# Optimization experiments

Hardware: AMD Instinct MI355X
Metric: run time of the kernel (lower is better)

The kernel has to match this reference:

```python
import jax, jax.numpy as jnp
import numpy as np

N = 100000   # num_embeddings
D = 128      # embedding_dims
E = 128      # edge_output_size
S = 2048     # number of streaming interactions
W_DECAY = 1.0  # Decayer w, decay_method='exp': f(dt) = exp(-w*dt)


def setup_inputs() -> dict:
    key = jax.random.key(0)
    ks = jax.random.split(key, 20)
    def nrm(k, shape, s):
        return jax.random.normal(k, shape, jnp.float32) * s
    sD = 1.0 / np.sqrt(D)
    sE = 1.0 / np.sqrt(E)
    return {
        'heads': jax.random.randint(ks[0], (S,), 0, N, dtype=jnp.int32),
        'tails': jax.random.randint(ks[1], (S,), 0, N, dtype=jnp.int32),
        'times': jnp.sort(jax.random.uniform(ks[2], (S,), jnp.float32) * 100.0),
        # node state tables (nn.Embedding weights in the original)
        'node_rep': nrm(ks[3], (N, D), 0.1),
        'cell_head': nrm(ks[4], (N, D), 0.1),
        'hidden_head': nrm(ks[5], (N, D), 0.1),
        'cell_tail': nrm(ks[6], (N, D), 0.1),
        'hidden_tail': nrm(ks[7], (N, D), 0.1),
        # Edge_updater_nn head / tail: act(rep_h @ W1 + rep_t @ W2 + b)
        'Weh1': nrm(ks[8], (D, E), sD), 'Weh2': nrm(ks[9], (D, E), sD), 'beh': jnp.zeros((E,), jnp.float32),
        'Wet1': nrm(ks[10], (D, E), sD), 'Wet2': nrm(ks[11], (D, E), sD), 'bet': jnp.zeros((E,), jnp.float32),
        # TLSTM head (time-decayed LSTM cell)
        'Wxh': nrm(ks[12], (E, 4 * D), sE), 'Whh': nrm(ks[13], (D, 4 * D), sD), 'bh': jnp.zeros((4 * D,), jnp.float32),
        'Wdh': nrm(ks[14], (D, D), sD), 'bdh': jnp.zeros((D,), jnp.float32),
        # TLSTM tail
        'Wxt': nrm(ks[15], (E, 4 * D), sE), 'Wht': nrm(ks[16], (D, 4 * D), sD), 'bt': jnp.zeros((4 * D,), jnp.float32),
        'Wdt': nrm(ks[17], (D, D), sD), 'bdt': jnp.zeros((D,), jnp.float32),
        # Combiner: tanh(h_head @ Wc1 + h_tail @ Wc2)
        'Wc1': nrm(ks[18], (D, D), sD), 'Wc2': nrm(ks[19], (D, D), sD),
    }


def _tlstm(x, c, h, decay, Wx, Wh, b, Wd, bd):
    # Time-aware LSTM: decompose short-term memory, decay it by elapsed time, recombine.
    cs = jnp.tanh(c @ Wd + bd)      # short-term memory component
    c_adj = c - cs + cs * decay      # adjusted previous cell
    z = x @ Wx + h @ Wh + b          # [4D] gate pre-activations
    i, f, o, g = jnp.split(z, 4)
    i = jax.nn.sigmoid(i); f = jax.nn.sigmoid(f); o = jax.nn.sigmoid(o)
    g = jnp.tanh(g)
    c_new = f * c_adj + i * g
    h_new = o * jnp.tanh(c_new)
    return c_new, h_new


def reference(heads, tails, times, node_rep, cell_head, hidden_head, cell_tail, hidden_tail,
              Weh1, Weh2, beh, Wet1, Wet2, bet,
              Wxh, Whh, bh, Wdh, bdh, Wxt, Wht, bt, Wdt, bdt, Wc1, Wc2):
    recent = jnp.zeros((node_rep.shape[0],), jnp.float32)  # recent_timestamp, init 0

    def step(state, ev):
        rep, ch, hh, ct, ht, rt = state
        h_i, t_i, tm = ev
        rep_h = rep[h_i]                    # gather current reps
        rep_t = rep[t_i]
        dec_h = jnp.exp(-W_DECAY * (tm - rt[h_i]))   # decayer(delta_t)
        dec_t = jnp.exp(-W_DECAY * (tm - rt[t_i]))
        edge_h = jnp.tanh(rep_h @ Weh1 + rep_t @ Weh2 + beh)  # edge_updater_head
        edge_t = jnp.tanh(rep_h @ Wet1 + rep_t @ Wet2 + bet)  # edge_updater_tail
        c_h, h_h = _tlstm(edge_h, ch[h_i], hh[h_i], dec_h, Wxh, Whh, bh, Wdh, bdh)
        c_t, h_t = _tlstm(edge_t, ct[t_i], ht[t_i], dec_t, Wxt, Wht, bt, Wdt, bdt)
        new_rep_h = jnp.tanh(h_h @ Wc1 + ht[h_i] @ Wc2)  # combiner(head hidden, tail hidden)
        new_rep_t = jnp.tanh(hh[t_i] @ Wc1 + h_t @ Wc2)
        # scatter updated state (head written before tail, matching original ordering)
        rep = rep.at[h_i].set(new_rep_h).at[t_i].set(new_rep_t)
        ch = ch.at[h_i].set(c_h); hh = hh.at[h_i].set(h_h)
        ct = ct.at[t_i].set(c_t); ht = ht.at[t_i].set(h_t)
        rt = rt.at[h_i].set(tm).at[t_i].set(tm)
        # if_updated=0: emit pre-update representations for this interaction
        return (rep, ch, hh, ct, ht, rt), (rep_h, rep_t)

    state0 = (node_rep, cell_head, hidden_head, cell_tail, hidden_tail, recent)
    _, (out_h, out_t) = jax.lax.scan(step, state0, (heads, tails, times))
    return jnp.stack([out_h, out_t])  # [2, S, D]
```

## Files before the change

### kernel.cpp

```cpp
#include <hip/hip_runtime.h>
#include <hip/hip_cooperative_groups.h>
#include <math.h>

namespace cg = cooperative_groups;

#define NBLK 256
#define DD 128
#define SMAX 2048

__device__ __forceinline__ float sigmoidf(float x) { return 1.0f / (1.0f + expf(-x)); }

__global__ __launch_bounds__(1024) void schedule_kernel(
    const int* __restrict__ heads, const int* __restrict__ tails, int S,
    int* __restrict__ order, int* __restrict__ level_off, int* __restrict__ n_levels) {
  __shared__ int sh[SMAX], st[SMAX], lvl[SMAX], ph[SMAX], pt[SMAX], cnt[SMAX];
  __shared__ int changed, maxl;
  const int tid = threadIdx.x;

  for (int j = tid; j < S; j += 1024) { sh[j] = heads[j]; st[j] = tails[j]; }
  __syncthreads();

  for (int r = 0; r < 2; ++r) {
    int j = (r == 0) ? tid : (2047 - tid);
    if (j < S && (r == 0 ? (tid < 1024) : (2047 - tid >= 1024))) {
      int myh = sh[j], myt = st[j];
      int mph = -1, mpt = -1;
      for (int i = 0; i < j; ++i) {
        int a = sh[i], b = st[i];
        if (a == myh || b == myh) mph = i;
        if (a == myt || b == myt) mpt = i;
      }
      ph[j] = mph; pt[j] = mpt; lvl[j] = 1;
    }
  }
  __syncthreads();

  for (int it = 0; it < S + 2; ++it) {
    __syncthreads();
    if (tid == 0) changed = 0;
    __syncthreads();
    for (int j = tid; j < S; j += 1024) {
      int l = 1;
      int a = ph[j]; if (a >= 0) l = lvl[a] + 1;
      int b = pt[j]; if (b >= 0) { int lb = lvl[b] + 1; if (lb > l) l = lb; }
      if (l != lvl[j]) { lvl[j] = l; changed = 1; }
    }
    __syncthreads();
    if (!changed) break;
  }

  if (tid == 0) maxl = 0;
  __syncthreads();
  for (int j = tid; j < S; j += 1024) atomicMax(&maxl, lvl[j]);
  __syncthreads();
  const int M = maxl;

  for (int l = tid; l < M; l += 1024) cnt[l] = 0;
  __syncthreads();
  for (int j = tid; j < S; j += 1024) atomicAdd(&cnt[lvl[j] - 1], 1);
  __syncthreads();
  if (tid == 0) {
    int run = 0;
    level_off[0] = 0;
    for (int l = 0; l < M; ++l) { run += cnt[l]; level_off[l + 1] = run; }
    n_levels[0] = M;
  }
  __syncthreads();

  for (int l = tid; l < M; l += 1024) cnt[l] = 0;
  __syncthreads();
  for (int j = tid; j < S; j += 1024) {
    int lv = lvl[j] - 1;
    int pos = level_off[lv] + atomicAdd(&cnt[lv], 1);
    order[pos] = j;
  }
}

struct PParams {
  const int* heads; const int* tails; const float* times;
  float* node_rep; float* cell_head; float* hidden_head; float* cell_tail; float* hidden_tail;
  const float* Weh1; const float* Weh2; const float* beh;
  const float* Wet1; const float* Wet2; const float* bet;
  const float* Wxh; const float* Whh; const float* bh; const float* Wdh; const float* bdh;
  const float* Wxt; const float* Wht; const float* bt; const float* Wdt; const float* bdt;
  const float* Wc1; const float* Wc2;
  float* out; float* rt;
  const int* order; const int* level_off; const int* n_levels;
  int S;
};

__global__ __launch_bounds__(256) void process_kernel(PParams p) {
  cg::grid_group grid = cg::this_grid();
  const int tid = threadIdx.x;

  __shared__ float repH[DD], repT[DD], cHs[DD], hHs[DD], cTs[DD], hTs[DD];
  __shared__ float htH[DD], hhT[DD];
  __shared__ float edgeH[DD], edgeT[DD], cadjH[DD], cadjT[DD];
  __shared__ float zH[512], zT[512];
  __shared__ float nhH[DD], nhT[DD];
  __shared__ float dec2[2], tmS;
  __shared__ int idx2[2];

  const int nlv = p.n_levels[0];
  for (int lv = 0; lv < nlv; ++lv) {
    const int beg = p.level_off[lv], end = p.level_off[lv + 1];
    for (int k = beg + blockIdx.x; k < end; k += gridDim.x) {
      __syncthreads();
      const int s = p.order[k];
      if (tid == 0) { idx2[0] = p.heads[s]; idx2[1] = p.tails[s]; tmS = p.times[s]; }
      __syncthreads();
      const int hI = idx2[0], tI = idx2[1];
      const float tm = tmS;
      if (tid < 2) dec2[tid] = expf(-(tm - p.rt[idx2[tid]]));

      if (tid < DD) {
        const int d = tid;
        const size_t o = (size_t)hI * DD + d;
        float r = p.node_rep[o];
        repH[d] = r; cHs[d] = p.cell_head[o]; hHs[d] = p.hidden_head[o];
        htH[d] = p.hidden_tail[o];
        p.out[(size_t)s * DD + d] = r;
      } else {
        const int d = tid - DD;
        const size_t o = (size_t)tI * DD + d;
        float r = p.node_rep[o];
        repT[d] = r; cTs[d] = p.cell_tail[o]; hTs[d] = p.hidden_tail[o];
        hhT[d] = p.hidden_head[o];
        p.out[(size_t)(p.S + s) * DD + d] = r;
      }
      __syncthreads();

      if (tid < DD) {
        const int e = tid;
        float ae = p.beh[e], ac = p.bdh[e];
#pragma unroll 4
        for (int d = 0; d < DD; ++d) {
          ae += repH[d] * p.Weh1[d * DD + e] + repT[d] * p.Weh2[d * DD + e];
          ac += cHs[d] * p.Wdh[d * DD + e];
        }
        edgeH[e] = tanhf(ae);
        float cs = tanhf(ac);
        cadjH[e] = cHs[e] - cs + cs * dec2[0];
      } else {
        const int e = tid - DD;
        float ae = p.bet[e], ac = p.bdt[e];
#pragma unroll 4
        for (int d = 0; d < DD; ++d) {
          ae += repH[d] * p.Wet1[d * DD + e] + repT[d] * p.Wet2[d * DD + e];
          ac += cTs[d] * p.Wdt[d * DD + e];
        }
        edgeT[e] = tanhf(ae);
        float cs = tanhf(ac);
        cadjT[e] = cTs[e] - cs + cs * dec2[1];
      }
      __syncthreads();

      {
        float a0 = p.bh[tid], a1 = p.bh[tid + 256];
        float b0 = p.bt[tid], b1 = p.bt[tid + 256];
#pragma unroll 2
        for (int d = 0; d < DD; ++d) {
          const float eh = edgeH[d], hh = hHs[d], et = edgeT[d], ht = hTs[d];
          a0 += eh * p.Wxh[d * 512 + tid]       + hh * p.Whh[d * 512 + tid];
          a1 += eh * p.Wxh[d * 512 + tid + 256] + hh * p.Whh[d * 512 + tid + 256];
          b0 += et * p.Wxt[d * 512 + tid]       + ht * p.Wht[d * 512 + tid];
          b1 += et * p.Wxt[d * 512 + tid + 256] + ht * p.Wht[d * 512 + tid + 256];
        }
        zH[tid] = a0; zH[tid + 256] = a1;
        zT[tid] = b0; zT[tid + 256] = b1;
      }
      __syncthreads();

      if (tid < DD) {
        const int e = tid;
        float ig = sigmoidf(zH[e]), fg = sigmoidf(zH[DD + e]);
        float og = sigmoidf(zH[256 + e]), gg = tanhf(zH[384 + e]);
        float c = fg * cadjH[e] + ig * gg;
        float h = og * tanhf(c);
        nhH[e] = h;
        p.cell_head[(size_t)hI * DD + e] = c;
        p.hidden_head[(size_t)hI * DD + e] = h;
      } else {
        const int e = tid - DD;
        float ig = sigmoidf(zT[e]), fg = sigmoidf(zT[DD + e]);
        float og = sigmoidf(zT[256 + e]), gg = tanhf(zT[384 + e]);
        float c = fg * cadjT[e] + ig * gg;
        float h = og * tanhf(c);
        nhT[e] = h;
        p.cell_tail[(size_t)tI * DD + e] = c;
        p.hidden_tail[(size_t)tI * DD + e] = h;
      }
      if (tid == 0) p.rt[hI] = tm;
      if (tid == 1) p.rt[tI] = tm;
      __syncthreads();

      if (tid < DD) {
        const int e = tid;
        float a = 0.f;
#pragma unroll 4
        for (int d = 0; d < DD; ++d)
          a += nhH[d] * p.Wc1[d * DD + e] + htH[d] * p.Wc2[d * DD + e];
        if (hI != tI) p.node_rep[(size_t)hI * DD + e] = tanhf(a);
      } else {
        const int e = tid - DD;
        float a = 0.f;
#pragma unroll 4
        for (int d = 0; d < DD; ++d)
          a += hhT[d] * p.Wc1[d * DD + e] + nhT[d] * p.Wc2[d * DD + e];
        p.node_rep[(size_t)tI * DD + e] = tanhf(a);
      }
    }
    __threadfence();
    grid.sync();
  }
}

extern "C" void kernel_launch(void* const* d_in, const int* in_sizes, int n_in,
                              void* d_out, int out_size, void* d_ws, size_t ws_size,
                              hipStream_t stream) {
  const int* heads = (const int*)d_in[0];
  const int* tails = (const int*)d_in[1];
  const float* times = (const float*)d_in[2];
  float* node_rep    = (float*)d_in[3];
  float* cell_head   = (float*)d_in[4];
  float* hidden_head = (float*)d_in[5];
  float* cell_tail   = (float*)d_in[6];
  float* hidden_tail = (float*)d_in[7];
  const float* Weh1 = (const float*)d_in[8];
  const float* Weh2 = (const float*)d_in[9];
  const float* beh  = (const float*)d_in[10];
  const float* Wet1 = (const float*)d_in[11];
  const float* Wet2 = (const float*)d_in[12];
  const float* bet  = (const float*)d_in[13];
  const float* Wxh  = (const float*)d_in[14];
  const float* Whh  = (const float*)d_in[15];
  const float* bh   = (const float*)d_in[16];
  const float* Wdh  = (const float*)d_in[17];
  const float* bdh  = (const float*)d_in[18];
  const float* Wxt  = (const float*)d_in[19];
  const float* Wht  = (const float*)d_in[20];
  const float* bt   = (const float*)d_in[21];
  const float* Wdt  = (const float*)d_in[22];
  const float* bdt  = (const float*)d_in[23];
  const float* Wc1  = (const float*)d_in[24];
  const float* Wc2  = (const float*)d_in[25];

  const int S = in_sizes[0];
  const int N = in_sizes[3] / DD;

  char* ws = (char*)d_ws;
  float* rt = (float*)ws;
  size_t rtBytes = (((size_t)N * 4) + 511) & ~(size_t)511;
  int* order     = (int*)(ws + rtBytes);
  int* level_off = order + SMAX;
  int* n_levels  = level_off + SMAX + 1;

  hipMemsetAsync(rt, 0, (size_t)N * 4, stream);
  schedule_kernel<<<1, 1024, 0, stream>>>(heads, tails, S, order, level_off, n_levels);

  PParams p;
  p.heads = heads; p.tails = tails; p.times = times;
  p.node_rep = node_rep; p.cell_head = cell_head; p.hidden_head = hidden_head;
  p.cell_tail = cell_tail; p.hidden_tail = hidden_tail;
  p.Weh1 = Weh1; p.Weh2 = Weh2; p.beh = beh;
  p.Wet1 = Wet1; p.Wet2 = Wet2; p.bet = bet;
  p.Wxh = Wxh; p.Whh = Whh; p.bh = bh; p.Wdh = Wdh; p.bdh = bdh;
  p.Wxt = Wxt; p.Wht = Wht; p.bt = bt; p.Wdt = Wdt; p.bdt = bdt;
  p.Wc1 = Wc1; p.Wc2 = Wc2;
  p.out = (float*)d_out; p.rt = rt;
  p.order = order; p.level_off = level_off; p.n_levels = n_levels;
  p.S = S;

  void* args[] = { (void*)&p };
  hipLaunchCooperativeKernel((const void*)process_kernel, dim3(NBLK), dim3(256),
                             args, 0, stream);
}
```

Before: 808.2 us.

## Parallelize predecessor search across blocks and size cooperative grid by occupancy

The O(S^2) predecessor search used to run inside a single 1024-thread block. It now runs in its own kernel with one 64-lane wavefront per interaction and a shuffle max-reduction. Level propagation moves into a separate finalize kernel that reads the predecessors from workspace. The cooperative process kernel's grid is now sized from CU count and occupancy, up to 1024 blocks, with fallbacks, so more interactions per level can run concurrently. This adds an extra kernel launch and host occupancy queries on every call.

```diff
diff --git a/kernel.cpp b/kernel.cpp
--- a/kernel.cpp
+++ b/kernel.cpp
@@ -4,39 +4,44 @@
 
 namespace cg = cooperative_groups;
 
-#define NBLK 256
+#define NBLK_MAX 1024
 #define DD 128
 #define SMAX 2048
 
 __device__ __forceinline__ float sigmoidf(float x) { return 1.0f / (1.0f + expf(-x)); }
 
-__global__ __launch_bounds__(1024) void schedule_kernel(
+__global__ __launch_bounds__(64) void pred_kernel(
     const int* __restrict__ heads, const int* __restrict__ tails, int S,
+    int* __restrict__ ph, int* __restrict__ pt) {
+  const int j = blockIdx.x;
+  if (j >= S) return;
+  const int myh = heads[j], myt = tails[j];
+  const int lane = threadIdx.x;
+  int mph = -1, mpt = -1;
+  for (int i = lane; i < j; i += 64) {
+    int a = heads[i], b = tails[i];
+    if (a == myh || b == myh) mph = i;
+    if (a == myt || b == myt) mpt = i;
+  }
+#pragma unroll
+  for (int off = 32; off > 0; off >>= 1) {
+    mph = max(mph, __shfl_down(mph, off));
+    mpt = max(mpt, __shfl_down(mpt, off));
+  }
+  if (lane == 0) { ph[j] = mph; pt[j] = mpt; }
+}
+
+__global__ __launch_bounds__(1024) void finalize_kernel(
+    int S, const int* __restrict__ phg, const int* __restrict__ ptg,
     int* __restrict__ order, int* __restrict__ level_off, int* __restrict__ n_levels) {
-  __shared__ int sh[SMAX], st[SMAX], lvl[SMAX], ph[SMAX], pt[SMAX], cnt[SMAX];
+  __shared__ int lvl[SMAX], ph[SMAX], pt[SMAX], cnt[SMAX];
   __shared__ int changed, maxl;
   const int tid = threadIdx.x;
 
-  for (int j = tid; j < S; j += 1024) { sh[j] = heads[j]; st[j] = tails[j]; }
-  __syncthreads();
-
-  for (int r = 0; r < 2; ++r) {
-    int j = (r == 0) ? tid : (2047 - tid);
-    if (j < S && (r == 0 ? (tid < 1024) : (2047 - tid >= 1024))) {
-      int myh = sh[j], myt = st[j];
-      int mph = -1, mpt = -1;
-      for (int i = 0; i < j; ++i) {
-        int a = sh[i], b = st[i];
-        if (a == myh || b == myh) mph = i;
-        if (a == myt || b == myt) mpt = i;
-      }
-      ph[j] = mph; pt[j] = mpt; lvl[j] = 1;
-    }
-  }
+  for (int j = tid; j < S; j += 1024) { ph[j] = phg[j]; pt[j] = ptg[j]; lvl[j] = 1; }
   __syncthreads();
 
   for (int it = 0; it < S + 2; ++it) {
-    __syncthreads();
     if (tid == 0) changed = 0;
     __syncthreads();
     for (int j = tid; j < S; j += 1024) {
@@ -47,6 +52,7 @@
     }
     __syncthreads();
     if (!changed) break;
+    __syncthreads();
   }
 
   if (tid == 0) maxl = 0;
@@ -101,7 +107,9 @@
   __shared__ float dec2[2], tmS;
   __shared__ int idx2[2];
 
-  const int nlv = p.n_levels[0];
+  int nlv = p.n_levels[0];
+  if (nlv < 0) nlv = 0;
+  if (nlv > SMAX) nlv = SMAX;
   for (int lv = 0; lv < nlv; ++lv) {
     const int beg = p.level_off[lv], end = p.level_off[lv + 1];
     for (int k = beg + blockIdx.x; k < end; k += gridDim.x) {
@@ -254,9 +262,12 @@
   int* order     = (int*)(ws + rtBytes);
   int* level_off = order + SMAX;
   int* n_levels  = level_off + SMAX + 1;
+  int* ph        = n_levels + 64;
+  int* pt        = ph + SMAX;
 
   hipMemsetAsync(rt, 0, (size_t)N * 4, stream);
-  schedule_kernel<<<1, 1024, 0, stream>>>(heads, tails, S, order, level_off, n_levels);
+  pred_kernel<<<S, 64, 0, stream>>>(heads, tails, S, ph, pt);
+  finalize_kernel<<<1, 1024, 0, stream>>>(S, ph, pt, order, level_off, n_levels);
 
   PParams p;
   p.heads = heads; p.tails = tails; p.times = times;
@@ -272,6 +283,24 @@
   p.S = S;
 
   void* args[] = { (void*)&p };
-  hipLaunchCooperativeKernel((const void*)process_kernel, dim3(NBLK), dim3(256),
-                             args, 0, stream);
+
+  int dev = 0; hipGetDevice(&dev);
+  int nCU = 0;
+  hipDeviceGetAttribute(&nCU, hipDeviceAttributeMultiprocessorCount, dev);
+  if (nCU <= 0) nCU = 256;
+  int maxBlkPerCU = 0;
+  hipOccupancyMaxActiveBlocksPerMultiprocessor(&maxBlkPerCU, process_kernel, 256, 0);
+  if (maxBlkPerCU < 1) maxBlkPerCU = 1;
+  long long cap = (long long)nCU * (long long)maxBlkPerCU;
+  int grid = (int)(cap < NBLK_MAX ? cap : NBLK_MAX);
+  if (grid < 1) grid = nCU;
+
+  hipError_t err = hipLaunchCooperativeKernel(process_kernel, dim3(grid), dim3(256),
+                                              args, 0, stream);
+  if (err != hipSuccess && grid > 512) {
+    err = hipLaunchCooperativeKernel(process_kernel, dim3(512), dim3(256), args, 0, stream);
+  }
+  if (err != hipSuccess && grid > 256) {
+    err = hipLaunchCooperativeKernel(process_kernel, dim3(256), dim3(256), args, 0, stream);
+  }
 }
```

Result: faster. 779.0 us (-3.6%).
